# Performance work log

Measured on AMD Instinct MI355X. Metric: run time of the kernel, lower is better.

Reference implementation:

```python
import jax, jax.numpy as jnp
import numpy as np

B_PARAM = 1.0
BAND_WIDTH = 0.5
LOSS_WEIGHT = 1.0
EPS_REL = 1e-5
EPS_NORM = 1e-12


def setup_inputs() -> dict:
    key = jax.random.key(0)
    k1, k2 = jax.random.split(key)
    images = jax.random.normal(k1, (1, 256, 96, 96), dtype=jnp.float32)
    gt = jax.random.normal(k2, (1, 256, 96, 96), dtype=jnp.float32)
    return {"images": images, "gt": gt}


def _cosine_raw_distance(i_feat, t_feat):
    # _create_using_dot_p: center both by mean of t over (n, h, w), L2-normalize
    # along channels, then pairwise dot products -> cosine distance in [0, 1].
    mean_t = jnp.mean(t_feat, axis=(0, 2, 3), keepdims=True)
    i_c = i_feat - mean_t
    t_c = t_feat - mean_t
    i_n = i_c / jnp.maximum(jnp.sqrt(jnp.sum(i_c * i_c, axis=1, keepdims=True)), EPS_NORM)
    t_n = t_c / jnp.maximum(jnp.sqrt(jnp.sum(t_c * t_c, axis=1, keepdims=True)), EPS_NORM)
    n, c, h, w = i_n.shape
    t_v = t_n.reshape(n, c, h * w)
    # dot[n, h, w, s] = sum_c i_n[n,c,h,w] * t_v[n,c,s]   (the conv2d 1x1 kernel trick)
    dot = jnp.einsum('nchw,ncs->nhws', i_n, t_v)
    dist = jnp.clip((1.0 - dot) / 2.0, 0.0, None)
    return dist  # [n, h, w, h*w]


def _cx_loss(i_feat, t_feat):
    raw = _cosine_raw_distance(i_feat, t_feat)                      # [n,h,w,s]
    # relative distance (Eq. 2): divide each row by its min over target positions
    rel = raw / (jnp.min(raw, axis=-1, keepdims=True) + EPS_REL)
    w = jnp.exp((B_PARAM - rel) / BAND_WIDTH)
    cx = w / jnp.sum(w, axis=-1, keepdims=True)                     # row softmax-like
    max_gt_sim = jnp.max(cx, axis=(1, 2))                           # [n, s]
    cs = jnp.mean(max_gt_sim, axis=1)                               # [n]
    loss = jnp.mean(-jnp.log(cs))
    return loss * LOSS_WEIGHT


def reference(images, gt):
    # use_vgg=False, crop_quarter=False, h*w <= max_1d_size**2 -> direct CX loss.
    return _cx_loss(images, gt)
```

## Files before the change

### kernel.cpp

```cpp
#include <hip/hip_runtime.h>
#include <hip/hip_bf16.h>

#define S 9216
#define C 256
#define NCT 6
#define NG  (NCT*8)
#define SCH 1152

typedef __bf16 bf16x8 __attribute__((ext_vector_type(8)));
typedef float f32x4 __attribute__((ext_vector_type(4)));
typedef unsigned short us8 __attribute__((ext_vector_type(8)));
typedef unsigned short us4 __attribute__((ext_vector_type(4)));

#define GLOAD_LDS16(g, l) __builtin_amdgcn_global_load_lds( \
    (const __attribute__((address_space(1))) void*)(g),     \
    (__attribute__((address_space(3))) void*)(l), 16, 0, 0)

#define A2C 2.8853900817779268f

__device__ __forceinline__ float bf2f(unsigned short u) {
    return __uint_as_float(((unsigned)u) << 16);
}
__device__ __forceinline__ unsigned short f2bfbits(float x) {
    __hip_bfloat16 h = __float2bfloat16(x);
    return *reinterpret_cast<unsigned short*>(&h);
}

__global__ __launch_bounds__(256) void k_mean(const float* __restrict__ gt,
                                              float* __restrict__ meanT) {
    const int c = blockIdx.x;
    const float* p = gt + (size_t)c * S;
    float s = 0.f;
    for (int i = threadIdx.x; i < S; i += 256) s += p[i];
    for (int m = 1; m < 64; m <<= 1) s += __shfl_xor(s, m, 64);
    __shared__ float red[4];
    if ((threadIdx.x & 63) == 0) red[threadIdx.x >> 6] = s;
    __syncthreads();
    if (threadIdx.x == 0)
        meanT[c] = (red[0] + red[1] + red[2] + red[3]) * (1.0f / S);
}

__global__ __launch_bounds__(256) void k_ssq(const float* __restrict__ img,
                                             const float* __restrict__ gt,
                                             const float* __restrict__ meanT,
                                             float* __restrict__ ssqP,
                                             float* __restrict__ rowmin,
                                             float* __restrict__ rowsum,
                                             float* __restrict__ colmaxLog) {
    __shared__ float sm[32];
    const int part = blockIdx.x & 7;
    const int sb   = blockIdx.x >> 3;
    const int t    = threadIdx.x;
    if (t < 32) sm[t] = meanT[part * 32 + t];
    const int s = sb * 256 + t;
    if (part == 0) {
        rowmin[s]    = __uint_as_float(0x7f800000u);
        rowsum[s]    = 0.f;
        colmaxLog[s] = 0.f;
    }
    __syncthreads();
    float si = 0.f, st = 0.f;
    #pragma unroll 8
    for (int k = 0; k < 32; ++k) {
        const int c = part * 32 + k;
        const float m  = sm[k];
        const float di = img[(size_t)c * S + s] - m;
        const float dt = gt [(size_t)c * S + s] - m;
        si += di * di;
        st += dt * dt;
    }
    ssqP[(size_t)part * S + s]       = si;
    ssqP[(size_t)(part + 8) * S + s] = st;
}

__global__ __launch_bounds__(256) void k_write(const float* __restrict__ img,
                                               const float* __restrict__ gt,
                                               const float* __restrict__ meanT,
                                               const float* __restrict__ ssqP,
                                               __hip_bfloat16* __restrict__ A,
                                               __hip_bfloat16* __restrict__ B) {
    __shared__ float sm[32];
    const int part = blockIdx.x & 7;
    const int sb   = blockIdx.x >> 3;
    const int t    = threadIdx.x;
    if (t < 32) sm[t] = meanT[part * 32 + t];
    __syncthreads();
    const int s = sb * 256 + t;
    float si = 0.f, st = 0.f;
    #pragma unroll
    for (int p = 0; p < 8; ++p) {
        si += ssqP[(size_t)p * S + s];
        st += ssqP[(size_t)(p + 8) * S + s];
    }
    const float ri = 1.0f / fmaxf(sqrtf(si), 1e-12f);
    const float rt = 1.0f / fmaxf(sqrtf(st), 1e-12f);
    const int c0 = part * 32;
    #pragma unroll
    for (int cc = 0; cc < 4; ++cc) {
        us8 va, vb;
        #pragma unroll
        for (int e = 0; e < 8; ++e) {
            const int c = c0 + cc * 8 + e;
            const float m = sm[cc * 8 + e];
            va[e] = f2bfbits((img[(size_t)c * S + s] - m) * ri);
            vb[e] = f2bfbits((gt [(size_t)c * S + s] - m) * rt);
        }
        *reinterpret_cast<us8*>(A + (size_t)s * C + c0 + cc * 8) = va;
        *reinterpret_cast<us8*>(B + (size_t)s * C + c0 + cc * 8) = vb;
    }
}

__global__ __launch_bounds__(256, 2) void k_gemm_store(const __hip_bfloat16* __restrict__ A,
                                                       const __hip_bfloat16* __restrict__ B,
                                                       float* __restrict__ rowmin,
                                                       __hip_bfloat16* __restrict__ Q) {
    __shared__ alignas(16) __hip_bfloat16 As[64 * 256];
    __shared__ alignas(16) __hip_bfloat16 Bs[4 * 3 * 2048];
    const int tid  = threadIdx.x;
    const int lane = tid & 63;
    const int wid  = tid >> 6;
    const int orig = blockIdx.x;
    const int xcd  = orig & 7;
    const int q    = orig >> 3;
    const int colGroup = q / 18;
    const int strip    = xcd * 18 + (q % 18);
    const int rowBase = strip * 64;
    const int cb0     = colGroup * 1536;

    const int frow = lane & 15;
    const int kgrp = lane >> 4;

    {
        const int arow_lo = lane >> 5;
        const int achunk  = lane & 31;
        #pragma unroll
        for (int j = 0; j < 8; ++j) {
            const int row = wid * 16 + j * 2 + arow_lo;
            const int cc  = achunk ^ (row & 7);
            GLOAD_LDS16(A + (size_t)(rowBase + row) * C + cc * 8,
                        &As[(wid * 16 + j * 2) * 256 + lane * 8]);
        }
    }

    const int bcol4  = lane >> 2;
    const int bchunk = (lane & 3) ^ ((lane >> 3) & 3);
    __hip_bfloat16* const BsW = &Bs[wid * 6144];
    const __hip_bfloat16* const Bsrc = B + (size_t)(cb0 + wid * 64) * C;

#define STAGE_B(tt, kk, bb) do {                                              \
    _Pragma("unroll")                                                         \
    for (int i_ = 0; i_ < 4; ++i_) {                                          \
        GLOAD_LDS16(Bsrc + (size_t)((tt) * 256 + i_ * 16 + bcol4) * C         \
                         + (kk) * 32 + bchunk * 8,                            \
                    &BsW[(bb) * 2048 + i_ * 512]);                            \
    } } while (0)

    STAGE_B(0, 0, 0);
    STAGE_B(0, 1, 1);
    STAGE_B(0, 2, 2);

    asm volatile("s_waitcnt vmcnt(12)" ::: "memory");
    __builtin_amdgcn_s_barrier();

    const int bswz = (kgrp ^ ((frow >> 1) & 3)) * 8;

    float vmin[4][4];
    #pragma unroll
    for (int m = 0; m < 4; ++m)
        #pragma unroll
        for (int qq = 0; qq < 4; ++qq) vmin[m][qq] = 1e30f;

    int b0 = 0;
    for (int t = 0; t < NCT; ++t) {
        f32x4 acc[4][4] = {};
        #pragma unroll
        for (int kt = 0; kt < 8; ++kt) {
            if (kt < 3) {
                if (t) asm volatile("s_waitcnt vmcnt(24)" ::: "memory");
                else   asm volatile("s_waitcnt vmcnt(8)"  ::: "memory");
            } else if (kt < 6) {
                asm volatile("s_waitcnt vmcnt(8)" ::: "memory");
            } else if (kt == 6) {
                if (t == NCT - 1) asm volatile("s_waitcnt vmcnt(4)" ::: "memory");
                else              asm volatile("s_waitcnt vmcnt(8)" ::: "memory");
            } else {
                if (t == NCT - 1) asm volatile("s_waitcnt vmcnt(0)" ::: "memory");
                else              asm volatile("s_waitcnt vmcnt(8)" ::: "memory");
            }

            int bufc = b0 + (kt % 3);
            if (bufc >= 3) bufc -= 3;

            bf16x8 af[4], bfr[4];
            #pragma unroll
            for (int m = 0; m < 4; ++m) {
                const int row = m * 16 + frow;
                const int p   = (kt * 4 + kgrp) ^ (frow & 7);
                af[m] = *reinterpret_cast<const bf16x8*>(&As[row * 256 + p * 8]);
            }
            #pragma unroll
            for (int n = 0; n < 4; ++n)
                bfr[n] = *reinterpret_cast<const bf16x8*>(
                    &BsW[bufc * 2048 + (n * 16 + frow) * 32 + bswz]);

            asm volatile("s_waitcnt lgkmcnt(0)" ::: "memory");
            __builtin_amdgcn_sched_barrier(0);

            if (kt <= 4) {
                STAGE_B(t, kt + 3, bufc);
            } else if (t + 1 < NCT) {
                STAGE_B(t + 1, kt - 5, bufc);
            }

            #pragma unroll
            for (int m = 0; m < 4; ++m)
                #pragma unroll
                for (int n = 0; n < 4; ++n)
                    acc[m][n] = __builtin_amdgcn_mfma_f32_16x16x32_bf16(af[m], bfr[n], acc[m][n], 0, 0, 0);
        }
        b0 += 2; if (b0 >= 3) b0 -= 3;

        const int colBase = cb0 + t * 256;
        #pragma unroll
        for (int n = 0; n < 4; ++n) {
            const int cg = colBase + wid * 64 + n * 16 + frow;
            #pragma unroll
            for (int m = 0; m < 4; ++m) {
                us4 pk;
                #pragma unroll
                for (int qq = 0; qq < 4; ++qq) {
                    const float raw = fmaxf(0.5f * (1.0f - acc[m][n][qq]), 0.0f);
                    vmin[m][qq] = fminf(vmin[m][qq], raw);
                    pk[qq] = f2bfbits(raw);
                }
                *reinterpret_cast<us4*>(Q + (size_t)cg * S + rowBase + m * 16 + kgrp * 4) = pk;
            }
        }
    }
#undef STAGE_B

    #pragma unroll
    for (int m = 0; m < 4; ++m)
        #pragma unroll
        for (int qq = 0; qq < 4; ++qq) {
            float v = vmin[m][qq];
            v = fminf(v, __shfl_xor(v, 1, 64));
            v = fminf(v, __shfl_xor(v, 2, 64));
            v = fminf(v, __shfl_xor(v, 4, 64));
            v = fminf(v, __shfl_xor(v, 8, 64));
            if (frow == 0)
                atomicMin((unsigned int*)&rowmin[rowBase + m * 16 + kgrp * 4 + qq],
                          __float_as_uint(v));
        }
}

__global__ __launch_bounds__(256) void k_rowsum(const __hip_bfloat16* __restrict__ Q,
                                                const float* __restrict__ rowmin,
                                                float* __restrict__ rowsum) {
    __shared__ float sBrN[64];
    __shared__ float srs[64];
    const int t  = threadIdx.x;
    const int r0 = (blockIdx.x >> 3) * 64;
    const int s0 = (blockIdx.x & 7) * SCH;
    if (t < 64) {
        sBrN[t] = -A2C / (rowmin[r0 + t] + 1e-5f);
        srs[t]  = 0.f;
    }
    __syncthreads();
    const int roct = (t & 7) * 8;
    const int ss   = t >> 3;
    float brn[8];
    #pragma unroll
    for (int j = 0; j < 8; ++j) brn[j] = sBrN[roct + j];
    const __hip_bfloat16* base = Q + r0 + roct;

    float sums[8] = {};
    #pragma unroll 4
    for (int i = 0; i < SCH / 32; ++i) {
        const int s = s0 + ss + i * 32;
        const us8 v = *reinterpret_cast<const us8*>(base + (size_t)s * S);
        #pragma unroll
        for (int j = 0; j < 8; ++j)
            sums[j] += exp2f(fmaf(brn[j], bf2f(v[j]), A2C));
    }
    #pragma unroll
    for (int j = 0; j < 8; ++j) {
        float x = sums[j];
        x += __shfl_xor(x, 8, 64);
        x += __shfl_xor(x, 16, 64);
        x += __shfl_xor(x, 32, 64);
        if ((t & 63) < 8) atomicAdd(&srs[roct + j], x);
    }
    __syncthreads();
    if (t < 64) atomicAdd(&rowsum[r0 + t], srs[t]);
}

__global__ __launch_bounds__(256) void k_colmax(const __hip_bfloat16* __restrict__ Q,
                                                const float* __restrict__ rowmin,
                                                const float* __restrict__ rowsum,
                                                float* __restrict__ colmaxLog) {
    __shared__ float sBrN[64];
    __shared__ float sCA[64];
    const int t  = threadIdx.x;
    const int r0 = (blockIdx.x >> 3) * 64;
    const int s0 = (blockIdx.x & 7) * SCH;
    if (t < 64) {
        sBrN[t] = -A2C / (rowmin[r0 + t] + 1e-5f);
        sCA[t]  = A2C + 64.0f - __log2f(rowsum[r0 + t]);
    }
    __syncthreads();
    const int roct = (t & 7) * 8;
    const int ss   = t >> 3;
    float brn[8], ca[8];
    #pragma unroll
    for (int j = 0; j < 8; ++j) { brn[j] = sBrN[roct + j]; ca[j] = sCA[roct + j]; }
    const __hip_bfloat16* base = Q + r0 + roct;

    #pragma unroll 4
    for (int i = 0; i < SCH / 32; ++i) {
        const int s = s0 + ss + i * 32;
        const us8 v = *reinterpret_cast<const us8*>(base + (size_t)s * S);
        float mx = -1e30f;
        #pragma unroll
        for (int j = 0; j < 8; ++j)
            mx = fmaxf(mx, fmaf(brn[j], bf2f(v[j]), ca[j]));
        mx = fmaxf(mx, __shfl_xor(mx, 1, 64));
        mx = fmaxf(mx, __shfl_xor(mx, 2, 64));
        mx = fmaxf(mx, __shfl_xor(mx, 4, 64));
        if ((t & 7) == 0)
            atomicMax((unsigned int*)&colmaxLog[s], __float_as_uint(fmaxf(mx, 0.0f)));
    }
}

__global__ __launch_bounds__(256) void k_final(const float* __restrict__ colmaxLog,
                                               float* __restrict__ out) {
    float s = 0.f;
    for (int i = threadIdx.x; i < S; i += 256) s += exp2f(colmaxLog[i]);
    for (int m = 1; m < 64; m <<= 1) s += __shfl_xor(s, m, 64);
    __shared__ float red[4];
    if ((threadIdx.x & 63) == 0) red[threadIdx.x >> 6] = s;
    __syncthreads();
    if (threadIdx.x == 0) {
        const float total = red[0] + red[1] + red[2] + red[3];
        out[0] = -logf(total * (5.421010862427522e-20f / (float)S));
    }
}

extern "C" void kernel_launch(void* const* d_in, const int* in_sizes, int n_in,
                              void* d_out, int out_size, void* d_ws, size_t ws_size,
                              hipStream_t stream) {
    const float* img = (const float*)d_in[0];
    const float* gt  = (const float*)d_in[1];

    float* ws        = (float*)d_ws;
    float* meanT     = ws;
    float* rowmin    = ws + 256;
    float* rowsum    = rowmin + S;
    float* colmaxLog = rowsum + S;
    __hip_bfloat16* A = (__hip_bfloat16*)(colmaxLog + S);
    __hip_bfloat16* B = A + (size_t)S * C;
    __hip_bfloat16* Q = B + (size_t)S * C;
    float* ssqP = (float*)Q;
    float* out = (float*)d_out;

    k_mean <<<C, 256, 0, stream>>>(gt, meanT);
    k_ssq  <<<288, 256, 0, stream>>>(img, gt, meanT, ssqP, rowmin, rowsum, colmaxLog);
    k_write<<<288, 256, 0, stream>>>(img, gt, meanT, ssqP, A, B);

    k_gemm_store<<<864, 256, 0, stream>>>(A, B, rowmin, Q);
    k_rowsum<<<1152, 256, 0, stream>>>(Q, rowmin, rowsum);
    k_colmax<<<1152, 256, 0, stream>>>(Q, rowmin, rowsum, colmaxLog);

    k_final<<<1, 256, 0, stream>>>(colmaxLog, out);
}
```

Before: 214.7 us.

## Load A fragments directly to registers, drop A LDS tile, raise occupancy

The GEMM kernel no longer stages the 64x256 A strip in shared memory. Each wave now loads its A fragments straight from global memory into double-buffered registers, prefetching two k-steps ahead. This cuts LDS use so three blocks fit per CU, and the per-block column range shrinks (NCT 6→4, 1296 blocks) to spread work further. It also wraps the MFMAs in s_setprio. The cost is redundant global/L2 reads of A across the four waves and more VGPR pressure under the tighter launch bound.

```diff
diff --git a/kernel.cpp b/kernel.cpp
--- a/kernel.cpp
+++ b/kernel.cpp
@@ -3,7 +3,7 @@
 
 #define S 9216
 #define C 256
-#define NCT 6
+#define NCT 4
 #define NG  (NCT*8)
 #define SCH 1152
 
@@ -110,11 +110,10 @@
     }
 }
 
-__global__ __launch_bounds__(256, 2) void k_gemm_store(const __hip_bfloat16* __restrict__ A,
+__global__ __launch_bounds__(256, 3) void k_gemm_store(const __hip_bfloat16* __restrict__ A,
                                                        const __hip_bfloat16* __restrict__ B,
                                                        float* __restrict__ rowmin,
                                                        __hip_bfloat16* __restrict__ Q) {
-    __shared__ alignas(16) __hip_bfloat16 As[64 * 256];
     __shared__ alignas(16) __hip_bfloat16 Bs[4 * 3 * 2048];
     const int tid  = threadIdx.x;
     const int lane = tid & 63;
@@ -125,27 +124,16 @@
     const int colGroup = q / 18;
     const int strip    = xcd * 18 + (q % 18);
     const int rowBase = strip * 64;
-    const int cb0     = colGroup * 1536;
+    const int cb0     = colGroup * 1024;
 
     const int frow = lane & 15;
     const int kgrp = lane >> 4;
-
-    {
-        const int arow_lo = lane >> 5;
-        const int achunk  = lane & 31;
-        #pragma unroll
-        for (int j = 0; j < 8; ++j) {
-            const int row = wid * 16 + j * 2 + arow_lo;
-            const int cc  = achunk ^ (row & 7);
-            GLOAD_LDS16(A + (size_t)(rowBase + row) * C + cc * 8,
-                        &As[(wid * 16 + j * 2) * 256 + lane * 8]);
-        }
-    }
 
     const int bcol4  = lane >> 2;
     const int bchunk = (lane & 3) ^ ((lane >> 3) & 3);
     __hip_bfloat16* const BsW = &Bs[wid * 6144];
-    const __hip_bfloat16* const Bsrc = B + (size_t)(cb0 + wid * 64) * C;
+    const __hip_bfloat16* const Bsrc  = B + (size_t)(cb0 + wid * 64) * C;
+    const __hip_bfloat16* const Abase = A + (size_t)(rowBase + frow) * C + kgrp * 8;
 
 #define STAGE_B(tt, kk, bb) do {                                              \
     _Pragma("unroll")                                                         \
@@ -155,13 +143,20 @@
                     &BsW[(bb) * 2048 + i_ * 512]);                            \
     } } while (0)
 
+#define LOAD_AF(dst, kk) do {                                                 \
+    _Pragma("unroll")                                                         \
+    for (int m_ = 0; m_ < 4; ++m_)                                            \
+        dst[m_] = *reinterpret_cast<const bf16x8*>(                           \
+            Abase + (size_t)(m_ * 16) * C + (kk) * 32);                       \
+    } while (0)
+
+    bf16x8 afA[4], afB[4];
+    LOAD_AF(afA, 0);
+    LOAD_AF(afB, 1);
     STAGE_B(0, 0, 0);
     STAGE_B(0, 1, 1);
     STAGE_B(0, 2, 2);
 
-    asm volatile("s_waitcnt vmcnt(12)" ::: "memory");
-    __builtin_amdgcn_s_barrier();
-
     const int bswz = (kgrp ^ ((frow >> 1) & 3)) * 8;
 
     float vmin[4][4];
@@ -175,29 +170,18 @@
         f32x4 acc[4][4] = {};
         #pragma unroll
         for (int kt = 0; kt < 8; ++kt) {
-            if (kt < 3) {
-                if (t) asm volatile("s_waitcnt vmcnt(24)" ::: "memory");
-                else   asm volatile("s_waitcnt vmcnt(8)"  ::: "memory");
-            } else if (kt < 6) {
-                asm volatile("s_waitcnt vmcnt(8)" ::: "memory");
-            } else if (kt == 6) {
-                if (t == NCT - 1) asm volatile("s_waitcnt vmcnt(4)" ::: "memory");
-                else              asm volatile("s_waitcnt vmcnt(8)" ::: "memory");
-            } else {
-                if (t == NCT - 1) asm volatile("s_waitcnt vmcnt(0)" ::: "memory");
-                else              asm volatile("s_waitcnt vmcnt(8)" ::: "memory");
-            }
+            const int g = t * 8 + kt;
+            if (t == 0 && kt == 0)      asm volatile("s_waitcnt vmcnt(8)"  ::: "memory");
+            else if (t == 0 && kt == 1) asm volatile("s_waitcnt vmcnt(12)" ::: "memory");
+            else if (kt < 2)            asm volatile("s_waitcnt vmcnt(24)" ::: "memory");
+            else if (g == NG - 2)       asm volatile("s_waitcnt vmcnt(4)"  ::: "memory");
+            else if (g == NG - 1)       asm volatile("s_waitcnt vmcnt(0)"  ::: "memory");
+            else                        asm volatile("s_waitcnt vmcnt(8)"  ::: "memory");
 
             int bufc = b0 + (kt % 3);
             if (bufc >= 3) bufc -= 3;
 
-            bf16x8 af[4], bfr[4];
-            #pragma unroll
-            for (int m = 0; m < 4; ++m) {
-                const int row = m * 16 + frow;
-                const int p   = (kt * 4 + kgrp) ^ (frow & 7);
-                af[m] = *reinterpret_cast<const bf16x8*>(&As[row * 256 + p * 8]);
-            }
+            bf16x8 bfr[4];
             #pragma unroll
             for (int n = 0; n < 4; ++n)
                 bfr[n] = *reinterpret_cast<const bf16x8*>(
@@ -212,11 +196,26 @@
                 STAGE_B(t + 1, kt - 5, bufc);
             }
 
-            #pragma unroll
-            for (int m = 0; m < 4; ++m)
+            __builtin_amdgcn_s_setprio(1);
+            if (kt & 1) {
                 #pragma unroll
-                for (int n = 0; n < 4; ++n)
-                    acc[m][n] = __builtin_amdgcn_mfma_f32_16x16x32_bf16(af[m], bfr[n], acc[m][n], 0, 0, 0);
+                for (int m = 0; m < 4; ++m)
+                    #pragma unroll
+                    for (int n = 0; n < 4; ++n)
+                        acc[m][n] = __builtin_amdgcn_mfma_f32_16x16x32_bf16(afB[m], bfr[n], acc[m][n], 0, 0, 0);
+            } else {
+                #pragma unroll
+                for (int m = 0; m < 4; ++m)
+                    #pragma unroll
+                    for (int n = 0; n < 4; ++n)
+                        acc[m][n] = __builtin_amdgcn_mfma_f32_16x16x32_bf16(afA[m], bfr[n], acc[m][n], 0, 0, 0);
+            }
+            __builtin_amdgcn_s_setprio(0);
+
+            if (g <= NG - 3) {
+                if (kt & 1) LOAD_AF(afB, (kt + 2) & 7);
+                else        LOAD_AF(afA, (kt + 2) & 7);
+            }
         }
         b0 += 2; if (b0 >= 3) b0 -= 3;
 
@@ -238,6 +237,7 @@
         }
     }
 #undef STAGE_B
+#undef LOAD_AF
 
     #pragma unroll
     for (int m = 0; m < 4; ++m)
@@ -367,7 +367,7 @@
     k_ssq  <<<288, 256, 0, stream>>>(img, gt, meanT, ssqP, rowmin, rowsum, colmaxLog);
     k_write<<<288, 256, 0, stream>>>(img, gt, meanT, ssqP, A, B);
 
-    k_gemm_store<<<864, 256, 0, stream>>>(A, B, rowmin, Q);
+    k_gemm_store<<<1296, 256, 0, stream>>>(A, B, rowmin, Q);
     k_rowsum<<<1152, 256, 0, stream>>>(Q, rowmin, rowsum);
     k_colmax<<<1152, 256, 0, stream>>>(Q, rowmin, rowsum, colmaxLog);
 
```

After: 329.4 us. 53.4% more time.

## Fuse rowsum and colmax passes into one per-row-strip sweep kernel

Applied to the files above, without the earlier changes.

Merges the separate rowsum and colmax kernels into a single kernel in which each block owns a 32-row strip across all columns. The block first computes the row sums in shared memory, then re-reads its strip to compute the column maxima. This removes a launch, the global rowsum buffer and its atomics, and should make the second read of Q hit in cache. In exchange the grid drops from 1152 to 288 blocks, each looping over 9216 columns serially, which lowers parallelism and adds two block barriers.

```diff
diff --git a/kernel.cpp b/kernel.cpp
--- a/kernel.cpp
+++ b/kernel.cpp
@@ -5,7 +5,6 @@
 #define C 256
 #define NCT 6
 #define NG  (NCT*8)
-#define SCH 1152
 
 typedef __bf16 bf16x8 __attribute__((ext_vector_type(8)));
 typedef float f32x4 __attribute__((ext_vector_type(4)));
@@ -45,7 +44,6 @@
                                              const float* __restrict__ meanT,
                                              float* __restrict__ ssqP,
                                              float* __restrict__ rowmin,
-                                             float* __restrict__ rowsum,
                                              float* __restrict__ colmaxLog) {
     __shared__ float sm[32];
     const int part = blockIdx.x & 7;
@@ -55,7 +53,6 @@
     const int s = sb * 256 + t;
     if (part == 0) {
         rowmin[s]    = __uint_as_float(0x7f800000u);
-        rowsum[s]    = 0.f;
         colmaxLog[s] = 0.f;
     }
     __syncthreads();
@@ -141,7 +138,6 @@
                         &As[(wid * 16 + j * 2) * 256 + lane * 8]);
         }
     }
-
     const int bcol4  = lane >> 2;
     const int bchunk = (lane & 3) ^ ((lane >> 3) & 3);
     __hip_bfloat16* const BsW = &Bs[wid * 6144];
@@ -254,30 +250,29 @@
         }
 }
 
-__global__ __launch_bounds__(256) void k_rowsum(const __hip_bfloat16* __restrict__ Q,
-                                                const float* __restrict__ rowmin,
-                                                float* __restrict__ rowsum) {
-    __shared__ float sBrN[64];
-    __shared__ float srs[64];
+__global__ __launch_bounds__(512) void k_sweep(const __hip_bfloat16* __restrict__ Q,
+                                               const float* __restrict__ rowmin,
+                                               float* __restrict__ colmaxLog) {
+    __shared__ float sBrN[32];
+    __shared__ float srs[32];
+    __shared__ float sCA[32];
     const int t  = threadIdx.x;
-    const int r0 = (blockIdx.x >> 3) * 64;
-    const int s0 = (blockIdx.x & 7) * SCH;
-    if (t < 64) {
+    const int r0 = blockIdx.x * 32;
+    if (t < 32) {
         sBrN[t] = -A2C / (rowmin[r0 + t] + 1e-5f);
         srs[t]  = 0.f;
     }
     __syncthreads();
-    const int roct = (t & 7) * 8;
-    const int ss   = t >> 3;
+    const int g    = t & 3;
+    const int roct = g * 8;
+    const int ss   = t >> 2;
     float brn[8];
     #pragma unroll
     for (int j = 0; j < 8; ++j) brn[j] = sBrN[roct + j];
     const __hip_bfloat16* base = Q + r0 + roct;
 
     float sums[8] = {};
-    #pragma unroll 4
-    for (int i = 0; i < SCH / 32; ++i) {
-        const int s = s0 + ss + i * 32;
+    for (int s = ss; s < S; s += 128) {
         const us8 v = *reinterpret_cast<const us8*>(base + (size_t)s * S);
         #pragma unroll
         for (int j = 0; j < 8; ++j)
@@ -286,39 +281,20 @@
     #pragma unroll
     for (int j = 0; j < 8; ++j) {
         float x = sums[j];
+        x += __shfl_xor(x, 4, 64);
         x += __shfl_xor(x, 8, 64);
         x += __shfl_xor(x, 16, 64);
         x += __shfl_xor(x, 32, 64);
-        if ((t & 63) < 8) atomicAdd(&srs[roct + j], x);
-    }
-    __syncthreads();
-    if (t < 64) atomicAdd(&rowsum[r0 + t], srs[t]);
-}
-
-__global__ __launch_bounds__(256) void k_colmax(const __hip_bfloat16* __restrict__ Q,
-                                                const float* __restrict__ rowmin,
-                                                const float* __restrict__ rowsum,
-                                                float* __restrict__ colmaxLog) {
-    __shared__ float sBrN[64];
-    __shared__ float sCA[64];
-    const int t  = threadIdx.x;
-    const int r0 = (blockIdx.x >> 3) * 64;
-    const int s0 = (blockIdx.x & 7) * SCH;
-    if (t < 64) {
-        sBrN[t] = -A2C / (rowmin[r0 + t] + 1e-5f);
-        sCA[t]  = A2C + 64.0f - __log2f(rowsum[r0 + t]);
-    }
-    __syncthreads();
-    const int roct = (t & 7) * 8;
-    const int ss   = t >> 3;
-    float brn[8], ca[8];
-    #pragma unroll
-    for (int j = 0; j < 8; ++j) { brn[j] = sBrN[roct + j]; ca[j] = sCA[roct + j]; }
-    const __hip_bfloat16* base = Q + r0 + roct;
-
-    #pragma unroll 4
-    for (int i = 0; i < SCH / 32; ++i) {
-        const int s = s0 + ss + i * 32;
+        if ((t & 63) < 4) atomicAdd(&srs[roct + j], x);
+    }
+    __syncthreads();
+    if (t < 32) sCA[t] = A2C + 64.0f - __log2f(srs[t]);
+    __syncthreads();
+
+    float ca[8];
+    #pragma unroll
+    for (int j = 0; j < 8; ++j) ca[j] = sCA[roct + j];
+    for (int s = ss; s < S; s += 128) {
         const us8 v = *reinterpret_cast<const us8*>(base + (size_t)s * S);
         float mx = -1e30f;
         #pragma unroll
@@ -326,8 +302,7 @@
             mx = fmaxf(mx, fmaf(brn[j], bf2f(v[j]), ca[j]));
         mx = fmaxf(mx, __shfl_xor(mx, 1, 64));
         mx = fmaxf(mx, __shfl_xor(mx, 2, 64));
-        mx = fmaxf(mx, __shfl_xor(mx, 4, 64));
-        if ((t & 7) == 0)
+        if (g == 0)
             atomicMax((unsigned int*)&colmaxLog[s], __float_as_uint(fmaxf(mx, 0.0f)));
     }
 }
@@ -364,12 +339,11 @@
     float* out = (float*)d_out;
 
     k_mean <<<C, 256, 0, stream>>>(gt, meanT);
-    k_ssq  <<<288, 256, 0, stream>>>(img, gt, meanT, ssqP, rowmin, rowsum, colmaxLog);
+    k_ssq  <<<288, 256, 0, stream>>>(img, gt, meanT, ssqP, rowmin, colmaxLog);
     k_write<<<288, 256, 0, stream>>>(img, gt, meanT, ssqP, A, B);
 
     k_gemm_store<<<864, 256, 0, stream>>>(A, B, rowmin, Q);
-    k_rowsum<<<1152, 256, 0, stream>>>(Q, rowmin, rowsum);
-    k_colmax<<<1152, 256, 0, stream>>>(Q, rowmin, rowsum, colmaxLog);
+    k_sweep<<<288, 512, 0, stream>>>(Q, rowmin, colmaxLog);
 
     k_final<<<1, 256, 0, stream>>>(colmaxLog, out);
 }
```

Measured after the change: 248.7 us. +15.8%, slower.
